# Performance work log

Measured on AMD Instinct MI355X. Metric: run time of the kernel, lower is better.

## Reference

```python
import jax, jax.numpy as jnp
import numpy as np

H = 768
NH = 12
HD = 64
R = 4
SCALING = 8.0 / 4.0  # lora_alpha / r


def setup_inputs() -> dict:
    key = jax.random.key(0)
    ks = jax.random.split(key, 16)
    B, T = 16, 512
    s = 0.02
    x = jax.random.normal(ks[0], (B, T, H), dtype=jnp.float32)
    mask = jax.random.randint(ks[1], (B, T), 0, 2, dtype=jnp.int32)
    return {
        "x": x,
        "mask": mask,
        "Wq": jax.random.normal(ks[2], (H, H), jnp.float32) * s,
        "bq": jnp.zeros((H,), jnp.float32),
        "Aq": jax.random.normal(ks[3], (R, H), jnp.float32) * s,
        "Bq": jax.random.normal(ks[4], (H, R), jnp.float32) * s,
        "Wk": jax.random.normal(ks[5], (H, H), jnp.float32) * s,
        "bk": jnp.zeros((H,), jnp.float32),
        "Wv": jax.random.normal(ks[6], (H, H), jnp.float32) * s,
        "bv": jnp.zeros((H,), jnp.float32),
        "Av": jax.random.normal(ks[7], (R, H), jnp.float32) * s,
        "Bv": jax.random.normal(ks[8], (H, R), jnp.float32) * s,
        "Wo": jax.random.normal(ks[9], (H, H), jnp.float32) * s,
        "bo": jnp.zeros((H,), jnp.float32),
    }


def _lora_linear(x, W, b, A, Bm):
    # base: x @ W^T + b ; lora: (x @ A^T) @ B^T * scaling (dropout inactive at eval)
    return x @ W.T + b + (x @ A.T) @ Bm.T * SCALING


def reference(x, mask, Wq, bq, Aq, Bq, Wk, bk, Wv, bv, Av, Bv, Wo, bo):
    B, T, _ = x.shape
    q = _lora_linear(x, Wq, bq, Aq, Bq).reshape(B, T, NH, HD).transpose(0, 2, 1, 3)
    k = (x @ Wk.T + bk).reshape(B, T, NH, HD).transpose(0, 2, 1, 3)
    v = _lora_linear(x, Wv, bv, Av, Bv).reshape(B, T, NH, HD).transpose(0, 2, 1, 3)
    # [B, NH, T, T]
    scores = jnp.einsum("bhqd,bhkd->bhqk", q, k) / jnp.sqrt(jnp.float32(HD))
    m = (mask == 0)[:, None, None, :]  # mask key positions where mask==0
    scores = jnp.where(m, jnp.float32(-1e9), scores)
    attn = jax.nn.softmax(scores, axis=-1)  # dropout inactive at eval
    out = jnp.einsum("bhqk,bhkd->bhqd", attn, v)
    out = out.transpose(0, 2, 1, 3).reshape(B, T, H)
    return out @ Wo.T + bo
```

## Files before the change

kernel.cpp:

```cpp
#include <hip/hip_runtime.h>
#include <stdint.h>

#define H 768
#define NHEAD 12
#define HDIM 64
#define BATCH 16
#define TSEQ 512
#define BT (BATCH*TSEQ)
#define C3 (3*H)

typedef __attribute__((ext_vector_type(8))) short short8;
typedef __attribute__((ext_vector_type(4))) float floatx4;
typedef unsigned short u16;

__device__ __forceinline__ u16 f2bf(float f) {
    union { float f; unsigned int u; } v; v.f = f;
    unsigned int u = v.u;
    return (u16)((u + 0x7FFFu + ((u >> 16) & 1u)) >> 16);
}

__device__ __forceinline__ void async_ld16(const void* g, void* l) {
    __builtin_amdgcn_global_load_lds((__attribute__((address_space(1))) void*)g,
                                     (__attribute__((address_space(3))) void*)l,
                                     16, 0, 0);
}

#define PREP_BLOCKS 9216
#define CVT_BLOCKS  6144
#define CMP_BLOCKS  16
__global__ void prep_kernel(const float* __restrict__ Wq, const float* __restrict__ bq,
                            const float* __restrict__ Aq, const float* __restrict__ Bq,
                            const float* __restrict__ Wk, const float* __restrict__ bk,
                            const float* __restrict__ Wv, const float* __restrict__ bv,
                            const float* __restrict__ Av, const float* __restrict__ Bv,
                            const float* __restrict__ Wo, const float* __restrict__ x,
                            const int* __restrict__ mask,
                            u16* __restrict__ Wall, u16* __restrict__ Wobf,
                            float* __restrict__ bias_all, u16* __restrict__ xb,
                            u16* __restrict__ tokl, int* __restrict__ nvalid)
{
    const int bid = blockIdx.x;
    if (bid >= PREP_BLOCKS + CVT_BLOCKS) {
        const int b = bid - (PREP_BLOCKS + CVT_BLOCKS);
        if (threadIdx.x >= 64) return;
        const int lane = threadIdx.x;
        int base = 0;
        for (int t0 = 0; t0 < TSEQ; t0 += 64) {
            const int mv = mask[b*TSEQ + t0 + lane];
            const unsigned long long bal = __ballot(mv != 0);
            if (mv != 0) {
                const int pre = __popcll(bal & ((1ull << lane) - 1ull));
                tokl[b*TSEQ + base + pre] = (u16)(t0 + lane);
            }
            base += __popcll(bal);
        }
        if (lane == 0) nvalid[b] = base;
        for (int i = base + lane; i < TSEQ; i += 64) tokl[b*TSEQ + i] = 0;
        return;
    }
    if (bid >= PREP_BLOCKS) {
        const int i = ((bid - PREP_BLOCKS) * 256 + threadIdx.x) * 4;
        const float4 v = *(const float4*)(x + i);
        u16 o[4] = { f2bf(v.x), f2bf(v.y), f2bf(v.z), f2bf(v.w) };
        *(uint2*)(xb + i) = *(const uint2*)o;
        return;
    }
    const int idx = bid * 256 + threadIdx.x;
    const int r = idx / H;
    const int c = idx - r * H;
    if (r < H) {
        float v = Wq[idx] + 2.0f * (Bq[r*4+0]*Aq[c] + Bq[r*4+1]*Aq[H+c] +
                                    Bq[r*4+2]*Aq[2*H+c] + Bq[r*4+3]*Aq[3*H+c]);
        Wall[idx] = f2bf(v);
    } else if (r < 2*H) {
        Wall[idx] = f2bf(Wk[idx - H*H]);
    } else if (r < 3*H) {
        const int rr = r - 2*H;
        float v = Wv[rr*H + c] + 2.0f * (Bv[rr*4+0]*Av[c] + Bv[rr*4+1]*Av[H+c] +
                                         Bv[rr*4+2]*Av[2*H+c] + Bv[rr*4+3]*Av[3*H+c]);
        Wall[idx] = f2bf(v);
    } else {
        Wobf[idx - 3*H*H] = f2bf(Wo[idx - 3*H*H]);
    }
    if (idx < C3) {
        bias_all[idx] = (idx < H) ? bq[idx] : (idx < 2*H ? bk[idx - H] : bv[idx - 2*H]);
    }
}

template<int MODE, int TM, int NB, int MB, int MAP, int G>
__device__ __forceinline__
void gemm_body(const int j, const u16* __restrict__ A, const u16* __restrict__ Bw,
               const float* __restrict__ bias, void* __restrict__ Cout,
               const u16* __restrict__ tokl, const int* __restrict__ nvalid,
               const int K, const int ldc, u16* __restrict__ Ablk, u16* __restrict__ Bblk)
{
    constexpr int MT = TM / 32;
    const int tid  = threadIdx.x;
    const int wave = tid >> 6;
    const int lane = tid & 63;
    const int quad = lane >> 4;
    const int l16  = lane & 15;

    int m0, n0;
    {
        const int xcd = j & 7;
        const int loc = j >> 3;
        if (MAP == 0) {
            constexpr int Mx = MB / 8;
            const int dm = loc % Mx;
            const int nb = loc / Mx;
            m0 = (xcd + 8*dm) * TM;
            n0 = nb * 128;
        } else {
            const int dm = loc % MB;
            const int nl = loc / MB;
            m0 = dm * TM;
            n0 = (xcd + 8*nl) * 128;
        }
    }

    if (G == 1) {
        const int b = n0 >> 9;
        if ((n0 & 511) >= ((nvalid[b] + 31) & ~31)) return;
    }
    if (G == 2) {
        const int b = m0 >> 9;
        if ((m0 & 511) >= ((nvalid[b] + 31) & ~31)) return;
    }

    const int mw = (wave & 1) * (TM / 2);
    const int nw = (wave >> 1) * 64;

    const int r8 = lane >> 3;
    const int kgs = ((lane & 7) ^ r8) * 8;
    const u16* gA = A  + (size_t)(m0 + wave*(TM/4) + r8) * K + kgs;
    const u16* gB = Bw + (size_t)(n0 + wave*32      + r8) * K + kgs;
    const u16* gAp[MT];
    const u16* gBp[4];
    if (G == 2) {
        #pragma unroll
        for (int jj = 0; jj < MT; jj++) {
            const int rs = m0 + wave*(TM/4) + jj*8 + r8;
            const int row = (rs & ~511) + (int)tokl[rs];
            gAp[jj] = A + (size_t)row * K + kgs;
        }
    }
    if (G == 1) {
        #pragma unroll
        for (int jj = 0; jj < 4; jj++) {
            const int rb = n0 + wave*32 + jj*8 + r8;
            const int row = (rb & ~511) + (int)tokl[rb];
            gBp[jj] = Bw + (size_t)row * K + kgs;
        }
    }
    u16* lA = Ablk + wave * (TM/4) * 64;
    u16* lB = Bblk + wave * 32 * 64;

    floatx4 acc[MT][4] = {};
    const int sw = l16 & 7;

    for (int k0 = 0; k0 < K; k0 += 64) {
        __syncthreads();
        #pragma unroll
        for (int jj = 0; jj < MT; jj++) {
            if (G == 2) async_ld16(gAp[jj] + k0, lA + jj*8*64);
            else        async_ld16(gA + k0 + (size_t)(jj*8) * K, lA + jj*8*64);
        }
        #pragma unroll
        for (int jj = 0; jj < 4; jj++) {
            if (G == 1) async_ld16(gBp[jj] + k0, lB + jj*8*64);
            else        async_ld16(gB + k0 + (size_t)(jj*8) * K, lB + jj*8*64);
        }
        __syncthreads();
        #pragma unroll
        for (int kk = 0; kk < 2; kk++) {
            short8 af[MT], bfr[4];
            #pragma unroll
            for (int mt = 0; mt < MT; mt++)
                af[mt] = *(const short8*)(Ablk + (mw + mt*16 + l16)*64 + ((quad + 4*kk) ^ sw)*8);
            #pragma unroll
            for (int nt = 0; nt < 4; nt++)
                bfr[nt] = *(const short8*)(Bblk + (nw + nt*16 + l16)*64 + ((quad + 4*kk) ^ sw)*8);
            #pragma unroll
            for (int mt = 0; mt < MT; mt++)
                #pragma unroll
                for (int nt = 0; nt < 4; nt++)
                    acc[mt][nt] = __builtin_amdgcn_mfma_f32_16x16x32_bf16(af[mt], bfr[nt], acc[mt][nt], 0, 0, 0);
        }
    }

    if (MODE == 2) {
        #pragma unroll
        for (int mt = 0; mt < MT; mt++) {
            #pragma unroll
            for (int r = 0; r < 4; r++) {
                const int m  = m0 + mw + mt*16 + quad*4 + r;
                const float bv = bias[m];
                const int hh = m >> 6, d = m & 63;
                #pragma unroll
                for (int nt = 0; nt < 4; nt++) {
                    const int n = n0 + nw + nt*16 + l16;
                    const int b = n >> 9, t = n & 511;
                    ((u16*)Cout)[((size_t)((b*NHEAD + hh)*HDIM + d))*TSEQ + t]
                        = f2bf(acc[mt][nt][r] + bv);
                }
            }
        }
    } else {
        #pragma unroll
        for (int nt = 0; nt < 4; nt++) {
            const int n = n0 + nw + nt*16 + l16;
            const float bv = bias[n];
            #pragma unroll
            for (int mt = 0; mt < MT; mt++) {
                #pragma unroll
                for (int r = 0; r < 4; r++) {
                    const int m = m0 + mw + mt*16 + quad*4 + r;
                    const float v = acc[mt][nt][r] + bv;
                    if (MODE == 1) ((u16*)Cout)[(size_t)m * ldc + n] = f2bf(v);
                    else           ((float*)Cout)[(size_t)m * ldc + n] = v;
                }
            }
        }
    }
}

template<int MODE, int TM, int NB, int MB, int MAP, int G>
__global__ __launch_bounds__(256)
void gemm_bt(const u16* __restrict__ A, const u16* __restrict__ Bw,
             const float* __restrict__ bias, void* __restrict__ Cout,
             const u16* __restrict__ tokl, const int* __restrict__ nvalid,
             int K, int ldc)
{
    __shared__ u16 Ablk[TM * 64];
    __shared__ u16 Bblk[128 * 64];
    gemm_body<MODE,TM,NB,MB,MAP,G>(blockIdx.x, A, Bw, bias, Cout, tokl, nvalid,
                                   K, ldc, Ablk, Bblk);
}

__global__ __launch_bounds__(256)
void gemm_qkv(const u16* __restrict__ xb, const u16* __restrict__ Wall,
              const float* __restrict__ biasall,
              u16* __restrict__ qb, u16* __restrict__ kc, u16* __restrict__ vt,
              const u16* __restrict__ tokl, const int* __restrict__ nvalid)
{
    __shared__ u16 Ablk[128 * 64];
    __shared__ u16 Bblk[128 * 64];
    const int bid = blockIdx.x;
    if (bid < 384) {
        gemm_body<1,128,6,64,0,0>(bid, xb, Wall, biasall, qb,
                                  nullptr, nullptr, H, H, Ablk, Bblk);
    } else if (bid < 1152) {
        gemm_body<1,64,6,128,0,2>(bid - 384, xb, Wall + (size_t)H*H, biasall + H, kc,
                                  tokl, nvalid, H, H, Ablk, Bblk);
    } else {
        gemm_body<2,64,64,12,1,1>(bid - 1152, Wall + (size_t)2*H*H, xb, biasall + 2*H, vt,
                                  tokl, nvalid, H, 0, Ablk, Bblk);
    }
}

#define PSTRIDE 40

__global__ __launch_bounds__(256)
void attn_kernel(const u16* __restrict__ qb, const u16* __restrict__ kc,
                 const u16* __restrict__ vt, const int* __restrict__ nvalid,
                 u16* __restrict__ attn_out)
{
    __shared__ float maskadd[TSEQ];
    __shared__ u16 Kbuf[2][32 * 64];
    __shared__ u16 Vbuf[2][64 * 32];
    __shared__ u16 Pbuf[4][2][16 * PSTRIDE];

    const int qt = blockIdx.x;
    const int bh = blockIdx.y;
    const int b = bh / NHEAD, h = bh - b * NHEAD;
    const int tid  = threadIdx.x;
    const int wave = tid >> 6;
    const int lane = tid & 63;
    const int quad = lane >> 4;
    const int l16  = lane & 15;

    const int nv = nvalid[b];
    const int nt = (nv + 31) >> 5;

    for (int i = tid; i < TSEQ; i += 256)
        maskadd[i] = (i < nv) ? 0.0f : -1e9f;

    const size_t btok = (size_t)b * TSEQ;
    const int q0 = qt * 128 + wave * 32;

    short8 qf[2][2];
    #pragma unroll
    for (int m = 0; m < 2; m++) {
        const u16* qp = qb + (btok + q0 + m*16 + l16) * H + h*HDIM + quad*8;
        qf[m][0] = *(const short8*)qp;
        qf[m][1] = *(const short8*)(qp + 32);
    }

    const u16* kglob = kc + btok * H + h*HDIM;
    const u16* vglob = vt + (size_t)bh * HDIM * TSEQ;

    auto stage = [&](int kb, int pp) {
        {
            const int r = lane >> 3;
            const int g = (lane & 7) ^ r;
            async_ld16(kglob + (size_t)(kb + wave*8 + r) * H + g*8,
                       &Kbuf[pp][wave*8*64]);
        }
        {
            const int dr = lane >> 2;
            const int g  = (lane & 3) ^ ((dr >> 1) & 3);
            async_ld16(vglob + (size_t)(wave*16 + dr) * TSEQ + kb + g*8,
                       &Vbuf[pp][wave*16*32]);
        }
    };

    floatx4 o[2][4] = {};
    float lsum[2][4] = {};

    auto compute = [&](int kb, int pp) {
        const u16* Kb_ = Kbuf[pp];
        const u16* Vb_ = Vbuf[pp];
        short8 kf[2][2];
        #pragma unroll
        for (int t = 0; t < 2; t++)
            #pragma unroll
            for (int h2 = 0; h2 < 2; h2++)
                kf[t][h2] = *(const short8*)(Kb_ + (t*16 + l16)*64 + (((h2*4 + quad) ^ (l16 & 7))*8));
        short8 vf[4];
        #pragma unroll
        for (int dt = 0; dt < 4; dt++)
            vf[dt] = *(const short8*)(Vb_ + (dt*16 + l16)*32 + ((quad ^ ((l16 >> 1) & 3))*8));

        floatx4 s[2][2];
        #pragma unroll
        for (int m = 0; m < 2; m++)
            #pragma unroll
            for (int t = 0; t < 2; t++) {
                floatx4 acc = {0.f, 0.f, 0.f, 0.f};
                acc = __builtin_amdgcn_mfma_f32_16x16x32_bf16(qf[m][0], kf[t][0], acc, 0, 0, 0);
                acc = __builtin_amdgcn_mfma_f32_16x16x32_bf16(qf[m][1], kf[t][1], acc, 0, 0, 0);
                s[m][t] = acc;
            }
        const float m0 = maskadd[kb + l16];
        const float m1 = maskadd[kb + 16 + l16];
        #pragma unroll
        for (int m = 0; m < 2; m++) {
            u16* Pw = Pbuf[wave][m];
            #pragma unroll
            for (int r = 0; r < 4; r++) {
                const float p0 = __expf(s[m][0][r] * 0.125f + m0);
                const float p1 = __expf(s[m][1][r] * 0.125f + m1);
                lsum[m][r] += p0 + p1;
                Pw[(quad*4 + r) * PSTRIDE + l16]      = f2bf(p0);
                Pw[(quad*4 + r) * PSTRIDE + 16 + l16] = f2bf(p1);
            }
        }
        #pragma unroll
        for (int m = 0; m < 2; m++) {
            const short8 pa = *(const short8*)(Pbuf[wave][m] + l16 * PSTRIDE + quad*8);
            #pragma unroll
            for (int dt = 0; dt < 4; dt++)
                o[m][dt] = __builtin_amdgcn_mfma_f32_16x16x32_bf16(pa, vf[dt], o[m][dt], 0, 0, 0);
        }
    };

    stage(0, 0);
    for (int it = 0; it < nt; it++) {
        __syncthreads();
        if (it < nt - 1) stage((it + 1) * 32, (it + 1) & 1);
        compute(it * 32, it & 1);
    }

    #pragma unroll
    for (int m = 0; m < 2; m++) {
        float inv[4];
        #pragma unroll
        for (int r = 0; r < 4; r++) {
            float l = lsum[m][r];
            l += __shfl_xor(l, 1);
            l += __shfl_xor(l, 2);
            l += __shfl_xor(l, 4);
            l += __shfl_xor(l, 8);
            inv[r] = 1.0f / l;
        }
        #pragma unroll
        for (int dt = 0; dt < 4; dt++)
            #pragma unroll
            for (int r = 0; r < 4; r++) {
                const int q = q0 + m*16 + quad*4 + r;
                attn_out[(btok + q) * H + h*HDIM + dt*16 + l16] = f2bf(o[m][dt][r] * inv[r]);
            }
    }
}

extern "C" void kernel_launch(void* const* d_in, const int* in_sizes, int n_in,
                              void* d_out, int out_size, void* d_ws, size_t ws_size,
                              hipStream_t stream)
{
    const float* x   = (const float*)d_in[0];
    const int* mask  = (const int*)d_in[1];
    const float* Wq  = (const float*)d_in[2];
    const float* bq  = (const float*)d_in[3];
    const float* Aq  = (const float*)d_in[4];
    const float* Bq  = (const float*)d_in[5];
    const float* Wk  = (const float*)d_in[6];
    const float* bk  = (const float*)d_in[7];
    const float* Wv  = (const float*)d_in[8];
    const float* bv  = (const float*)d_in[9];
    const float* Av  = (const float*)d_in[10];
    const float* Bv  = (const float*)d_in[11];
    const float* Wo  = (const float*)d_in[12];
    const float* bo  = (const float*)d_in[13];

    char* ws = (char*)d_ws;
    u16*   xb      = (u16*)  (ws);
    u16*   Wall    = (u16*)  (ws + 12582912);
    u16*   Wobf    = (u16*)  (ws + 16121856);
    float* biasall = (float*)(ws + 17301504);
    u16*   qb      = (u16*)  (ws + 17310720);
    u16*   kc      = (u16*)  (ws + 29893632);
    u16*   vt      = (u16*)  (ws + 42476544);
    u16*   attn_o  = (u16*)  (ws + 55059456);

    int* nvalid = (int*)((char*)d_out + 25149376);
    u16* tokl   = (u16*)((char*)d_out + 25149440);

    prep_kernel<<<PREP_BLOCKS + CVT_BLOCKS + CMP_BLOCKS, 256, 0, stream>>>(
        Wq, bq, Aq, Bq, Wk, bk, Wv, bv, Av, Bv, Wo, x, mask,
        Wall, Wobf, biasall, xb, tokl, nvalid);
    gemm_qkv<<<1920, 256, 0, stream>>>(xb, Wall, biasall, qb, kc, vt, tokl, nvalid);
    attn_kernel<<<dim3(TSEQ/128, BATCH*NHEAD), 256, 0, stream>>>(qb, kc, vt, nvalid, attn_o);
    gemm_bt<0,64,6,128,0,0><<<6*128, 256, 0, stream>>>(attn_o, Wobf, bo, d_out,
                                                       nullptr, nullptr, H, H);
}
```

Measured before the change: 189.6 us.

## Replace LDS-staged GEMM tiles with direct register loads and double buffering

```diff
diff --git a/kernel.cpp b/kernel.cpp
--- a/kernel.cpp
+++ b/kernel.cpp
@@ -92,8 +92,9 @@
 void gemm_body(const int j, const u16* __restrict__ A, const u16* __restrict__ Bw,
                const float* __restrict__ bias, void* __restrict__ Cout,
                const u16* __restrict__ tokl, const int* __restrict__ nvalid,
-               const int K, const int ldc, u16* __restrict__ Ablk, u16* __restrict__ Bblk)
-{
+               const int ldc)
+{
+    constexpr int K  = 768;
     constexpr int MT = TM / 32;
     const int tid  = threadIdx.x;
     const int wave = tid >> 6;
@@ -131,63 +132,48 @@
     const int mw = (wave & 1) * (TM / 2);
     const int nw = (wave >> 1) * 64;
 
-    const int r8 = lane >> 3;
-    const int kgs = ((lane & 7) ^ r8) * 8;
-    const u16* gA = A  + (size_t)(m0 + wave*(TM/4) + r8) * K + kgs;
-    const u16* gB = Bw + (size_t)(n0 + wave*32      + r8) * K + kgs;
-    const u16* gAp[MT];
-    const u16* gBp[4];
-    if (G == 2) {
-        #pragma unroll
-        for (int jj = 0; jj < MT; jj++) {
-            const int rs = m0 + wave*(TM/4) + jj*8 + r8;
-            const int row = (rs & ~511) + (int)tokl[rs];
-            gAp[jj] = A + (size_t)row * K + kgs;
-        }
-    }
-    if (G == 1) {
-        #pragma unroll
-        for (int jj = 0; jj < 4; jj++) {
-            const int rb = n0 + wave*32 + jj*8 + r8;
-            const int row = (rb & ~511) + (int)tokl[rb];
-            gBp[jj] = Bw + (size_t)row * K + kgs;
-        }
-    }
-    u16* lA = Ablk + wave * (TM/4) * 64;
-    u16* lB = Bblk + wave * 32 * 64;
+    const u16* pa[MT];
+    const u16* pb[4];
+    #pragma unroll
+    for (int mt = 0; mt < MT; mt++) {
+        int row = m0 + mw + mt*16 + l16;
+        if (G == 2) row = (row & ~511) + (int)tokl[row];
+        pa[mt] = A + (size_t)row * K + quad*8;
+    }
+    #pragma unroll
+    for (int nt = 0; nt < 4; nt++) {
+        int row = n0 + nw + nt*16 + l16;
+        if (G == 1) row = (row & ~511) + (int)tokl[row];
+        pb[nt] = Bw + (size_t)row * K + quad*8;
+    }
 
     floatx4 acc[MT][4] = {};
-    const int sw = l16 & 7;
-
+    short8 a0[MT], b0[4], a1[MT], b1[4];
+
+    #define LOADF(av, bv_, k0)                                            \
+        { _Pragma("unroll")                                               \
+          for (int mt = 0; mt < MT; mt++) av[mt] = *(const short8*)(pa[mt] + (k0)); \
+          _Pragma("unroll")                                               \
+          for (int nt = 0; nt < 4; nt++) bv_[nt] = *(const short8*)(pb[nt] + (k0)); }
+
+    #define STEPF(av, bv_)                                                \
+        { _Pragma("unroll")                                               \
+          for (int mt = 0; mt < MT; mt++)                                 \
+            _Pragma("unroll")                                             \
+            for (int nt = 0; nt < 4; nt++)                                \
+              acc[mt][nt] = __builtin_amdgcn_mfma_f32_16x16x32_bf16(av[mt], bv_[nt], acc[mt][nt], 0, 0, 0); }
+
+    LOADF(a0, b0, 0);
+    LOADF(a1, b1, 32);
+    #pragma unroll
     for (int k0 = 0; k0 < K; k0 += 64) {
-        __syncthreads();
-        #pragma unroll
-        for (int jj = 0; jj < MT; jj++) {
-            if (G == 2) async_ld16(gAp[jj] + k0, lA + jj*8*64);
-            else        async_ld16(gA + k0 + (size_t)(jj*8) * K, lA + jj*8*64);
-        }
-        #pragma unroll
-        for (int jj = 0; jj < 4; jj++) {
-            if (G == 1) async_ld16(gBp[jj] + k0, lB + jj*8*64);
-            else        async_ld16(gB + k0 + (size_t)(jj*8) * K, lB + jj*8*64);
-        }
-        __syncthreads();
-        #pragma unroll
-        for (int kk = 0; kk < 2; kk++) {
-            short8 af[MT], bfr[4];
-            #pragma unroll
-            for (int mt = 0; mt < MT; mt++)
-                af[mt] = *(const short8*)(Ablk + (mw + mt*16 + l16)*64 + ((quad + 4*kk) ^ sw)*8);
-            #pragma unroll
-            for (int nt = 0; nt < 4; nt++)
-                bfr[nt] = *(const short8*)(Bblk + (nw + nt*16 + l16)*64 + ((quad + 4*kk) ^ sw)*8);
-            #pragma unroll
-            for (int mt = 0; mt < MT; mt++)
-                #pragma unroll
-                for (int nt = 0; nt < 4; nt++)
-                    acc[mt][nt] = __builtin_amdgcn_mfma_f32_16x16x32_bf16(af[mt], bfr[nt], acc[mt][nt], 0, 0, 0);
-        }
-    }
+        STEPF(a0, b0);
+        if (k0 + 64 < K) LOADF(a0, b0, k0 + 64);
+        STEPF(a1, b1);
+        if (k0 + 96 < K) LOADF(a1, b1, k0 + 96);
+    }
+    #undef LOADF
+    #undef STEPF
 
     if (MODE == 2) {
         #pragma unroll
@@ -230,12 +216,9 @@
 void gemm_bt(const u16* __restrict__ A, const u16* __restrict__ Bw,
              const float* __restrict__ bias, void* __restrict__ Cout,
              const u16* __restrict__ tokl, const int* __restrict__ nvalid,
-             int K, int ldc)
-{
-    __shared__ u16 Ablk[TM * 64];
-    __shared__ u16 Bblk[128 * 64];
-    gemm_body<MODE,TM,NB,MB,MAP,G>(blockIdx.x, A, Bw, bias, Cout, tokl, nvalid,
-                                   K, ldc, Ablk, Bblk);
+             int ldc)
+{
+    gemm_body<MODE,TM,NB,MB,MAP,G>(blockIdx.x, A, Bw, bias, Cout, tokl, nvalid, ldc);
 }
 
 __global__ __launch_bounds__(256)
@@ -244,18 +227,16 @@
               u16* __restrict__ qb, u16* __restrict__ kc, u16* __restrict__ vt,
               const u16* __restrict__ tokl, const int* __restrict__ nvalid)
 {
-    __shared__ u16 Ablk[128 * 64];
-    __shared__ u16 Bblk[128 * 64];
     const int bid = blockIdx.x;
     if (bid < 384) {
         gemm_body<1,128,6,64,0,0>(bid, xb, Wall, biasall, qb,
-                                  nullptr, nullptr, H, H, Ablk, Bblk);
+                                  nullptr, nullptr, H);
     } else if (bid < 1152) {
         gemm_body<1,64,6,128,0,2>(bid - 384, xb, Wall + (size_t)H*H, biasall + H, kc,
-                                  tokl, nvalid, H, H, Ablk, Bblk);
+                                  tokl, nvalid, H);
     } else {
         gemm_body<2,64,64,12,1,1>(bid - 1152, Wall + (size_t)2*H*H, xb, biasall + 2*H, vt,
-                                  tokl, nvalid, H, 0, Ablk, Bblk);
+                                  tokl, nvalid, 0);
     }
 }
 
@@ -432,5 +413,5 @@
     gemm_qkv<<<1920, 256, 0, stream>>>(xb, Wall, biasall, qb, kc, vt, tokl, nvalid);
     attn_kernel<<<dim3(TSEQ/128, BATCH*NHEAD), 256, 0, stream>>>(qb, kc, vt, nvalid, attn_o);
     gemm_bt<0,64,6,128,0,0><<<6*128, 256, 0, stream>>>(attn_o, Wobf, bo, d_out,
-                                                       nullptr, nullptr, H, H);
-}
+                                                       nullptr, nullptr, H);
+}
```

Result: slower. 315.0 us (+66.2%).
